# Optimization experiments

Hardware: AMD Instinct MI355X
Metric: run time of the kernel (lower is better)

The kernel has to match this reference:

```python
import jax, jax.numpy as jnp
import numpy as np

D = 1024   # dim_embedding
H = 16     # n_head
HD = D // H


def setup_inputs() -> dict:
    key = jax.random.key(0)
    ks = jax.random.split(key, 5)
    B, T = 2, 2048
    x = jax.random.normal(ks[0], (B, T, D), dtype=jnp.float32)
    e = jax.random.normal(ks[1], (B, T, D), dtype=jnp.float32)
    s = 0.02
    W_en = jax.random.normal(ks[2], (D, 2 * D), dtype=jnp.float32) * s   # c_attn_en (k,v from encoder)
    W_q = jax.random.normal(ks[3], (D, D), dtype=jnp.float32) * s        # c_attn (q from decoder)
    W_o = jax.random.normal(ks[4], (D, D), dtype=jnp.float32) * s        # c_proj
    return {"x": x, "e": e, "W_en": W_en, "W_q": W_q, "W_o": W_o}


def reference(x, e, W_en, W_q, W_o):
    B, T, C = e.shape
    kv = e @ W_en                       # [B,T,2C]
    k, v = jnp.split(kv, 2, axis=-1)    # [B,T,C] each
    q = x @ W_q                         # [B,T,C]
    # reshape to heads: [B,H,T,hd]
    q = q.reshape(B, T, H, HD).transpose(0, 2, 1, 3)
    k = k.reshape(B, T, H, HD).transpose(0, 2, 1, 3)
    v = v.reshape(B, T, H, HD).transpose(0, 2, 1, 3)
    att = jnp.einsum("bhqd,bhkd->bhqk", q, k) * (1.0 / jnp.sqrt(jnp.float32(HD)))
    att = jax.nn.softmax(att, axis=-1)  # dropout=0 (eval)
    y = jnp.einsum("bhqk,bhkd->bhqd", att, v)
    y = y.transpose(0, 2, 1, 3).reshape(B, T, C)
    return y @ W_o
```

## Files before the change

kernel.cpp:

```cpp
#include <hip/hip_runtime.h>

typedef unsigned short u16;
typedef unsigned int u32;
typedef __bf16 bf16x8 __attribute__((ext_vector_type(8)));
typedef float f32x4 __attribute__((ext_vector_type(4)));
typedef float f32x16 __attribute__((ext_vector_type(16)));

#define D_EMB 1024
#define T_SEQ 2048
#define NH 16
#define HD 64

#define GLB(p) ((const __attribute__((address_space(1))) unsigned int*)(p))
#define LDSP(p) ((__attribute__((address_space(3))) unsigned int*)(p))

__device__ __forceinline__ u16 f2bf(float f) {
  union { float f; unsigned u; } c; c.f = f;
  unsigned u = c.u;
  unsigned r = (u + 0x7FFFu + ((u >> 16) & 1u)) >> 16;
  return (u16)r;
}
__device__ __forceinline__ u32 fbits(float f) {
  union { float f; unsigned u; } c; c.f = f; return c.u;
}

__global__ __launch_bounds__(256) void prep_kernel(
    const float* __restrict__ x, const float* __restrict__ e,
    const float* __restrict__ W_q, const float* __restrict__ W_en, const float* __restrict__ W_o,
    u16* __restrict__ xb, u16* __restrict__ eb,
    u16* __restrict__ Wqt, u16* __restrict__ Went, u16* __restrict__ Wot) {
  __shared__ float tile[32][33];
  const int bid = blockIdx.x, tid = threadIdx.x;
  if (bid < 8192) {
    const float* in = (bid < 4096) ? x : e;
    u16* out = (bid < 4096) ? xb : eb;
    int i = (bid & 4095) * 256 + tid;
    float4 v = reinterpret_cast<const float4*>(in)[i];
    ushort4 o;
    o.x = f2bf(v.x); o.y = f2bf(v.y); o.z = f2bf(v.z); o.w = f2bf(v.w);
    reinterpret_cast<ushort4*>(out)[i] = o;
    return;
  }
  const float* in; u16* out; int K, N, bx, by;
  int rem = bid - 8192;
  if (rem < 1024)      { in = W_q;  out = Wqt;  K = 1024; N = 1024; bx = rem & 31; by = rem >> 5; }
  else if (rem < 3072) { int r2 = rem - 1024; in = W_en; out = Went; K = 1024; N = 2048; bx = r2 & 63; by = r2 >> 6; }
  else                 { int r3 = rem - 3072; in = W_o;  out = Wot;  K = 1024; N = 1024; bx = r3 & 31; by = r3 >> 5; }
  int tx = tid & 31, ty = tid >> 5;
  int n0 = bx * 32, k0 = by * 32;
#pragma unroll
  for (int s = 0; s < 4; s++)
    tile[ty + 8 * s][tx] = in[(size_t)(k0 + ty + 8 * s) * N + n0 + tx];
  __syncthreads();
#pragma unroll
  for (int s = 0; s < 4; s++)
    out[(size_t)(n0 + ty + 8 * s) * K + k0 + tx] = f2bf(tile[tx][ty + 8 * s]);
}

__global__ __launch_bounds__(256) void proj_kernel(
    const u16* __restrict__ xb, const u16* __restrict__ eb,
    const u16* __restrict__ Wqt, const u16* __restrict__ Went,
    u16* __restrict__ qw, u16* __restrict__ kw, u16* __restrict__ vTw) {
  __shared__ u16 Al0[128 * 32], Bl0[128 * 32];
  __shared__ u16 Al1[128 * 32], Bl1[128 * 32];
  const int tid = threadIdx.x;
  const int nb = blockIdx.x, mb = blockIdx.y;
  const int wave = tid >> 6, lane = tid & 63;
  const int ln15 = lane & 15, quad = lane >> 4;
  const int wm = wave & 1, wn = wave >> 1;

  const u16* A = (nb < 8) ? xb : eb;
  const u16* Wt = (nb < 8) ? (Wqt + (size_t)nb * 128 * D_EMB)
                           : (Went + ((size_t)nb * 128 - D_EMB) * D_EMB);

  const int srow = lane >> 2, sch = lane & 3;
  const int gch = sch ^ ((srow >> 1) & 3);
  const u16* gA = A + (size_t)(mb * 128 + wave * 32 + srow) * D_EMB + gch * 8;
  const u16* gB = Wt + (size_t)(wave * 32 + srow) * D_EMB + gch * 8;

  auto stage = [&](int kb, u16* AL, u16* BL) {
    char* lA = (char*)AL + wave * 2048;
    char* lB = (char*)BL + wave * 2048;
#pragma unroll
    for (int it = 0; it < 2; it++) {
      __builtin_amdgcn_global_load_lds(GLB(gA + (size_t)it * 16 * D_EMB + kb), LDSP(lA + it * 1024), 16, 0, 0);
      __builtin_amdgcn_global_load_lds(GLB(gB + (size_t)it * 16 * D_EMB + kb), LDSP(lB + it * 1024), 16, 0, 0);
    }
  };

  f32x4 acc[4][4] = {};

  auto compute = [&](const u16* AL, const u16* BL) {
    bf16x8 af[4], bfr[4];
#pragma unroll
    for (int mt = 0; mt < 4; mt++) {
      int r = wm * 64 + mt * 16 + ln15;
      af[mt] = *reinterpret_cast<const bf16x8*>(&AL[r * 32 + ((quad ^ ((r >> 1) & 3)) * 8)]);
    }
#pragma unroll
    for (int nt = 0; nt < 4; nt++) {
      int r = wn * 64 + nt * 16 + ln15;
      bfr[nt] = *reinterpret_cast<const bf16x8*>(&BL[r * 32 + ((quad ^ ((r >> 1) & 3)) * 8)]);
    }
#pragma unroll
    for (int mt = 0; mt < 4; mt++)
#pragma unroll
      for (int nt = 0; nt < 4; nt++)
        acc[mt][nt] = __builtin_amdgcn_mfma_f32_16x16x32_bf16(af[mt], bfr[nt], acc[mt][nt], 0, 0, 0);
  };

  stage(0, Al0, Bl0);
  for (int kb = 0; kb < D_EMB; kb += 64) {
    __syncthreads();
    stage(kb + 32, Al1, Bl1);
    compute(Al0, Bl0);
    __syncthreads();
    if (kb + 64 < D_EMB) stage(kb + 64, Al0, Bl0);
    compute(Al1, Bl1);
  }

  const float QSCL = 0.125f * 1.44269504f;
#pragma unroll
  for (int mt = 0; mt < 4; mt++) {
#pragma unroll
    for (int nt = 0; nt < 4; nt++) {
#pragma unroll
      for (int i = 0; i < 4; i++) {
        int rr = mb * 128 + wm * 64 + mt * 16 + quad * 4 + i;
        int c  = nb * 128 + wn * 64 + nt * 16 + ln15;
        float v = acc[mt][nt][i];
        int b = rr >> 11, t = rr & 2047;
        if (c < D_EMB) {
          int h = c >> 6, d = c & 63;
          qw[(((size_t)(b * NH + h)) * T_SEQ + t) * HD + d] = f2bf(v * QSCL);
        } else if (c < 2 * D_EMB) {
          int cc = c - D_EMB; int h = cc >> 6, d = cc & 63;
          kw[(((size_t)(b * NH + h)) * T_SEQ + t) * HD + d] = f2bf(v);
        } else {
          int cc = c - 2 * D_EMB; int h = cc >> 6, d = cc & 63;
          vTw[(((size_t)(b * NH + h)) * HD + d) * T_SEQ + t] = f2bf(v);
        }
      }
    }
  }
}

__global__ __launch_bounds__(256) void attn_kernel(
    const u16* __restrict__ q, const u16* __restrict__ k,
    const u16* __restrict__ vT, u16* __restrict__ y) {
  __shared__ u16 Kl0[64][64], Vl0[64][64];
  __shared__ u16 Kl1[64][64], Vl1[64][64];
  __shared__ u16 Pl[4][32][64];

  const int bh = blockIdx.y;
  const int qt = blockIdx.x;
  const int tid = threadIdx.x;
  const int wave = tid >> 6, lane = tid & 63;
  const int q32 = lane & 31, hi = lane >> 5;
  const int b = bh >> 4, h = bh & 15;

  const int qrow = qt * 128 + wave * 32 + q32;
  const u16* qbase = q + ((size_t)bh * T_SEQ + qrow) * HD;
  bf16x8 qf[4];
#pragma unroll
  for (int s = 0; s < 4; s++)
    qf[s] = *reinterpret_cast<const bf16x8*>(qbase + s * 16 + hi * 8);

  f32x16 o2[2] = {};
  float lp = 0.f;

  const int srow = (lane >> 3) & 7;
  const int gch  = (lane & 7) ^ srow;
  const u16* kg0 = k  + ((size_t)bh * T_SEQ + wave * 16 + srow) * HD + gch * 8;
  const u16* vg0 = vT + ((size_t)bh * HD + wave * 16 + srow) * T_SEQ + gch * 8;

  auto issue_dma = [&](int t, u16 (*KL)[64], u16 (*VL)[64]) {
    char* klb = (char*)KL + wave * 2048;
    char* vlb = (char*)VL + wave * 2048;
    const u16* kp = kg0 + (size_t)t * 64 * HD;
    const u16* vp = vg0 + t * 64;
    __builtin_amdgcn_global_load_lds(GLB(kp),             LDSP(klb),        16, 0, 0);
    __builtin_amdgcn_global_load_lds(GLB(kp + 8 * HD),    LDSP(klb + 1024), 16, 0, 0);
    __builtin_amdgcn_global_load_lds(GLB(vp),             LDSP(vlb),        16, 0, 0);
    __builtin_amdgcn_global_load_lds(GLB(vp + 8 * T_SEQ), LDSP(vlb + 1024), 16, 0, 0);
  };

  auto body = [&](const u16 (*KL)[64], const u16 (*VL)[64]) {
    f32x16 s2[2] = {};
#pragma unroll
    for (int s = 0; s < 4; s++)
#pragma unroll
      for (int kt2 = 0; kt2 < 2; kt2++) {
        int r = kt2 * 32 + q32;
        bf16x8 kf = *reinterpret_cast<const bf16x8*>(&KL[r][(((s * 2 + hi) ^ (r & 7)) * 8)]);
        s2[kt2] = __builtin_amdgcn_mfma_f32_32x32x16_bf16(kf, qf[s], s2[kt2], 0, 0, 0);
      }

#pragma unroll
    for (int kt2 = 0; kt2 < 2; kt2++)
#pragma unroll
      for (int g = 0; g < 4; g++) {
        float p0 = __builtin_amdgcn_exp2f(s2[kt2][4 * g + 0]);
        float p1 = __builtin_amdgcn_exp2f(s2[kt2][4 * g + 1]);
        float p2 = __builtin_amdgcn_exp2f(s2[kt2][4 * g + 2]);
        float p3 = __builtin_amdgcn_exp2f(s2[kt2][4 * g + 3]);
        lp += (p0 + p1) + (p2 + p3);
        u32 dw0 = __builtin_amdgcn_perm(fbits(p1), fbits(p0), 0x07060302u);
        u32 dw1 = __builtin_amdgcn_perm(fbits(p3), fbits(p2), 0x07060302u);
        int phys = (kt2 * 4 + g) ^ (q32 & 7);
        *reinterpret_cast<uint2*>(&Pl[wave][q32][phys * 8 + 4 * hi]) = make_uint2(dw0, dw1);
      }
    asm volatile("s_waitcnt lgkmcnt(0)" ::: "memory");

#pragma unroll
    for (int s = 0; s < 4; s++) {
      bf16x8 pf = *reinterpret_cast<const bf16x8*>(
          &Pl[wave][q32][(((s * 2 + hi) ^ (q32 & 7)) * 8)]);
#pragma unroll
      for (int dt = 0; dt < 2; dt++) {
        int r = dt * 32 + q32;
        bf16x8 vf = *reinterpret_cast<const bf16x8*>(&VL[r][(((s * 2 + hi) ^ (r & 7)) * 8)]);
        o2[dt] = __builtin_amdgcn_mfma_f32_32x32x16_bf16(vf, pf, o2[dt], 0, 0, 0);
      }
    }
  };

  issue_dma(0, Kl0, Vl0);
  for (int t = 0; t < 32; t += 2) {
    __syncthreads();
    issue_dma(t + 1, Kl1, Vl1);
    body(Kl0, Vl0);
    __syncthreads();
    if (t + 2 < 32) issue_dma(t + 2, Kl0, Vl0);
    body(Kl1, Vl1);
  }

  lp += __shfl_xor(lp, 32, 64);
  const float inv = 1.0f / lp;

  const size_t ybase = ((size_t)b * T_SEQ + qrow) * D_EMB + h * 64;
#pragma unroll
  for (int dt = 0; dt < 2; dt++)
#pragma unroll
    for (int g = 0; g < 4; g++) {
      u16 b0 = f2bf(o2[dt][4 * g + 0] * inv), b1 = f2bf(o2[dt][4 * g + 1] * inv);
      u16 b2 = f2bf(o2[dt][4 * g + 2] * inv), b3 = f2bf(o2[dt][4 * g + 3] * inv);
      u32 dw0 = (u32)b0 | ((u32)b1 << 16);
      u32 dw1 = (u32)b2 | ((u32)b3 << 16);
      *reinterpret_cast<uint2*>(&y[ybase + dt * 32 + 8 * g + 4 * hi]) = make_uint2(dw0, dw1);
    }
}

__global__ __launch_bounds__(256) void oproj_kernel(
    const u16* __restrict__ yw, const u16* __restrict__ Wot, float* __restrict__ out) {
  __shared__ u16 Al0[64 * 32], Al1[64 * 32];
  __shared__ u16 Bl0[128 * 32], Bl1[128 * 32];
  const int tid = threadIdx.x;
  const int nb = blockIdx.x, mb = blockIdx.y;
  const int wave = tid >> 6, lane = tid & 63;
  const int ln15 = lane & 15, quad = lane >> 4;
  const int wm = wave & 1, wn = wave >> 1;

  const int srow = lane >> 2, sch = lane & 3;
  const int gch = sch ^ ((srow >> 1) & 3);
  const u16* gA = yw  + (size_t)(mb * 64 + wave * 16 + srow) * D_EMB + gch * 8;
  const u16* gB = Wot + (size_t)(nb * 128 + wave * 32 + srow) * D_EMB + gch * 8;

  auto stage = [&](int kb, u16* AL, u16* BL) {
    char* lA = (char*)AL + wave * 1024;
    char* lB = (char*)BL + wave * 2048;
    __builtin_amdgcn_global_load_lds(GLB(gA + kb), LDSP(lA), 16, 0, 0);
#pragma unroll
    for (int it = 0; it < 2; it++)
      __builtin_amdgcn_global_load_lds(GLB(gB + (size_t)it * 16 * D_EMB + kb), LDSP(lB + it * 1024), 16, 0, 0);
  };

  f32x4 acc[2][4] = {};

  auto compute = [&](const u16* AL, const u16* BL) {
    bf16x8 af[2], bfr[4];
#pragma unroll
    for (int mt = 0; mt < 2; mt++) {
      int r = wm * 32 + mt * 16 + ln15;
      af[mt] = *reinterpret_cast<const bf16x8*>(&AL[r * 32 + ((quad ^ ((r >> 1) & 3)) * 8)]);
    }
#pragma unroll
    for (int nt = 0; nt < 4; nt++) {
      int r = wn * 64 + nt * 16 + ln15;
      bfr[nt] = *reinterpret_cast<const bf16x8*>(&BL[r * 32 + ((quad ^ ((r >> 1) & 3)) * 8)]);
    }
#pragma unroll
    for (int mt = 0; mt < 2; mt++)
#pragma unroll
      for (int nt = 0; nt < 4; nt++)
        acc[mt][nt] = __builtin_amdgcn_mfma_f32_16x16x32_bf16(af[mt], bfr[nt], acc[mt][nt], 0, 0, 0);
  };

  stage(0, Al0, Bl0);
  for (int kb = 0; kb < D_EMB; kb += 64) {
    __syncthreads();
    stage(kb + 32, Al1, Bl1);
    compute(Al0, Bl0);
    __syncthreads();
    if (kb + 64 < D_EMB) stage(kb + 64, Al0, Bl0);
    compute(Al1, Bl1);
  }

#pragma unroll
  for (int mt = 0; mt < 2; mt++)
#pragma unroll
    for (int nt = 0; nt < 4; nt++)
#pragma unroll
      for (int i = 0; i < 4; i++) {
        int rr = mb * 64 + wm * 32 + mt * 16 + quad * 4 + i;
        int c  = nb * 128 + wn * 64 + nt * 16 + ln15;
        out[(size_t)rr * D_EMB + c] = acc[mt][nt][i];
      }
}

extern "C" void kernel_launch(void* const* d_in, const int* in_sizes, int n_in,
                              void* d_out, int out_size, void* d_ws, size_t ws_size,
                              hipStream_t stream) {
  const float* x    = (const float*)d_in[0];
  const float* e    = (const float*)d_in[1];
  const float* W_en = (const float*)d_in[2];
  const float* W_q  = (const float*)d_in[3];
  const float* W_o  = (const float*)d_in[4];
  float* out = (float*)d_out;

  char* w = (char*)d_ws;
  u16* xb   = (u16*)(w);
  u16* eb   = (u16*)(w + (8u  << 20));
  u16* Wqt  = (u16*)(w + (16u << 20));
  u16* Went = (u16*)(w + (18u << 20));
  u16* Wot  = (u16*)(w + (22u << 20));
  u16* qw   = (u16*)(w + (24u << 20));
  u16* kw   = (u16*)(w + (32u << 20));
  u16* vT   = (u16*)(w + (40u << 20));
  u16* yw   = (u16*)(w + (48u << 20));

  prep_kernel<<<12288, 256, 0, stream>>>(x, e, W_q, W_en, W_o, xb, eb, Wqt, Went, Wot);
  proj_kernel<<<dim3(24, 32), 256, 0, stream>>>(xb, eb, Wqt, Went, qw, kw, vT);
  attn_kernel<<<dim3(T_SEQ / 128, 32), 256, 0, stream>>>(qw, kw, vT, yw);
  oproj_kernel<<<dim3(8, 64), 256, 0, stream>>>(yw, Wot, out);
}
```

Baseline: 209.7 us.

## Keep softmax probabilities in registers by permuting K rows instead of LDS round-trip

Removes the per-wave LDS staging buffer for the P matrix. K rows are loaded in a permuted order (swapping bits 2 and 3 of the row index) so the QK^T MFMA accumulator layout lines up with the B-operand layout of the PV MFMA. The probabilities can then be packed straight into bf16x8 registers. This drops the LDS writes, the lgkmcnt wait and the LDS reads per tile, at the cost of relying on exact MFMA register-layout reasoning for correctness.

```diff
diff --git a/kernel.cpp b/kernel.cpp
--- a/kernel.cpp
+++ b/kernel.cpp
@@ -150,7 +150,6 @@
     const u16* __restrict__ vT, u16* __restrict__ y) {
   __shared__ u16 Kl0[64][64], Vl0[64][64];
   __shared__ u16 Kl1[64][64], Vl1[64][64];
-  __shared__ u16 Pl[4][32][64];
 
   const int bh = blockIdx.y;
   const int qt = blockIdx.x;
@@ -158,6 +157,9 @@
   const int wave = tid >> 6, lane = tid & 63;
   const int q32 = lane & 31, hi = lane >> 5;
   const int b = bh >> 4, h = bh & 15;
+
+  const int pq = (q32 & 19) | ((q32 & 8) >> 1) | ((q32 & 4) << 1);
+  const int pq7 = pq & 7;
 
   const int qrow = qt * 128 + wave * 32 + q32;
   const u16* qbase = q + ((size_t)bh * T_SEQ + qrow) * HD;
@@ -191,31 +193,31 @@
     for (int s = 0; s < 4; s++)
 #pragma unroll
       for (int kt2 = 0; kt2 < 2; kt2++) {
-        int r = kt2 * 32 + q32;
-        bf16x8 kf = *reinterpret_cast<const bf16x8*>(&KL[r][(((s * 2 + hi) ^ (r & 7)) * 8)]);
+        int r = kt2 * 32 + pq;
+        bf16x8 kf = *reinterpret_cast<const bf16x8*>(&KL[r][(((s * 2 + hi) ^ pq7) * 8)]);
         s2[kt2] = __builtin_amdgcn_mfma_f32_32x32x16_bf16(kf, qf[s], s2[kt2], 0, 0, 0);
       }
 
 #pragma unroll
-    for (int kt2 = 0; kt2 < 2; kt2++)
-#pragma unroll
-      for (int g = 0; g < 4; g++) {
-        float p0 = __builtin_amdgcn_exp2f(s2[kt2][4 * g + 0]);
-        float p1 = __builtin_amdgcn_exp2f(s2[kt2][4 * g + 1]);
-        float p2 = __builtin_amdgcn_exp2f(s2[kt2][4 * g + 2]);
-        float p3 = __builtin_amdgcn_exp2f(s2[kt2][4 * g + 3]);
-        lp += (p0 + p1) + (p2 + p3);
-        u32 dw0 = __builtin_amdgcn_perm(fbits(p1), fbits(p0), 0x07060302u);
-        u32 dw1 = __builtin_amdgcn_perm(fbits(p3), fbits(p2), 0x07060302u);
-        int phys = (kt2 * 4 + g) ^ (q32 & 7);
-        *reinterpret_cast<uint2*>(&Pl[wave][q32][phys * 8 + 4 * hi]) = make_uint2(dw0, dw1);
-      }
-    asm volatile("s_waitcnt lgkmcnt(0)" ::: "memory");
-
-#pragma unroll
     for (int s = 0; s < 4; s++) {
-      bf16x8 pf = *reinterpret_cast<const bf16x8*>(
-          &Pl[wave][q32][(((s * 2 + hi) ^ (q32 & 7)) * 8)]);
+      const int kt2 = s >> 1;
+      const int g0 = (2 * s) & 3;
+      float e0 = __builtin_amdgcn_exp2f(s2[kt2][4 * g0 + 0]);
+      float e1 = __builtin_amdgcn_exp2f(s2[kt2][4 * g0 + 1]);
+      float e2 = __builtin_amdgcn_exp2f(s2[kt2][4 * g0 + 2]);
+      float e3 = __builtin_amdgcn_exp2f(s2[kt2][4 * g0 + 3]);
+      float e4 = __builtin_amdgcn_exp2f(s2[kt2][4 * g0 + 4]);
+      float e5 = __builtin_amdgcn_exp2f(s2[kt2][4 * g0 + 5]);
+      float e6 = __builtin_amdgcn_exp2f(s2[kt2][4 * g0 + 6]);
+      float e7 = __builtin_amdgcn_exp2f(s2[kt2][4 * g0 + 7]);
+      lp += ((e0 + e1) + (e2 + e3)) + ((e4 + e5) + (e6 + e7));
+      u32 w0 = __builtin_amdgcn_perm(fbits(e1), fbits(e0), 0x07060302u);
+      u32 w1 = __builtin_amdgcn_perm(fbits(e3), fbits(e2), 0x07060302u);
+      u32 w2 = __builtin_amdgcn_perm(fbits(e5), fbits(e4), 0x07060302u);
+      u32 w3 = __builtin_amdgcn_perm(fbits(e7), fbits(e6), 0x07060302u);
+      union { u32 w[4]; bf16x8 v; } pu;
+      pu.w[0] = w0; pu.w[1] = w1; pu.w[2] = w2; pu.w[3] = w3;
+      bf16x8 pf = pu.v;
 #pragma unroll
       for (int dt = 0; dt < 2; dt++) {
         int r = dt * 32 + q32;
```

New measurement: 198.0 us. 1.06x faster.
